# Optimization experiments

Hardware: AMD Instinct MI355X
Metric: run time of the kernel (lower is better)

The kernel has to match this reference:

```python
import jax, jax.numpy as jnp
import numpy as np

N_NODES = 100000
N_EDGES = 3200000
D_IN = 256
D_OUT = 256


def setup_inputs() -> dict:
    key = jax.random.key(0)
    k1, k2, k3, k4, k5 = jax.random.split(key, 5)
    features = jax.random.normal(k1, (N_NODES, D_IN), dtype=jnp.float32)
    # xavier_uniform init for the weight
    limit = np.sqrt(6.0 / (D_IN + D_OUT)).astype(np.float32)
    weight = jax.random.uniform(k2, (D_IN, D_OUT), minval=-limit, maxval=limit, dtype=jnp.float32)
    adj_row = jax.random.randint(k3, (N_EDGES,), 0, N_NODES, dtype=jnp.int64)
    adj_col = jax.random.randint(k4, (N_EDGES,), 0, N_NODES, dtype=jnp.int64)
    adj_val = jax.random.uniform(k5, (N_EDGES,), dtype=jnp.float32)
    return {"features": features, "weight": weight, "adj_row": adj_row,
            "adj_col": adj_col, "adj_val": adj_val}


def reference(features, weight, adj_row, adj_col, adj_val):
    # support = features @ W   (dense GEMM)
    support = features @ weight                      # [N, D_OUT]
    # spmm: out[i] = sum_e val[e] * support[col[e]] for edges with row[e] == i
    gathered = adj_val[:, None] * support[adj_col]   # [E, D_OUT]
    out = jax.ops.segment_sum(gathered, adj_row, num_segments=features.shape[0])
    return jax.nn.relu(out)
```

## Files before the change

kernel.cpp:

```cpp
#include <hip/hip_runtime.h>
#include <hip/hip_bf16.h>

#define N_NODES 100000
#define N_EDGES 3200000
#define NBUCK   391

typedef short v8s __attribute__((ext_vector_type(8)));
typedef float v4f __attribute__((ext_vector_type(4)));

__device__ __forceinline__ unsigned short f2b(float x) {
    __hip_bfloat16 h = __float2bfloat16(x);
    return *reinterpret_cast<unsigned short*>(&h);
}
__device__ __forceinline__ float b2f(unsigned short u) {
    return __uint_as_float(((unsigned int)u) << 16);
}

__device__ __forceinline__ void gld16(const void* g, void* l) {
    __builtin_amdgcn_global_load_lds(
        (const __attribute__((address_space(1))) void*)g,
        (__attribute__((address_space(3))) void*)l, 16, 0, 0);
}

__global__ void transpose_b(const float* __restrict__ B, unsigned short* __restrict__ BT) {
    int n = blockIdx.x;
    int k = threadIdx.x;
    BT[n * 256 + k] = f2b(B[k * 256 + n]);
}

__global__ __launch_bounds__(512)
void gemm_dma(const float* __restrict__ A, const unsigned short* __restrict__ BT,
              unsigned short* __restrict__ C) {
    __shared__ __align__(16) float          sA[128 * 64];
    __shared__ __align__(16) unsigned short sB[256 * 64];

    const int tid  = threadIdx.x;
    const int wave = tid >> 6;
    const int lane = tid & 63;
    const int quad = lane >> 4;
    const int l16  = lane & 15;
    const int row0 = blockIdx.x * 128;

    v4f acc[16];
#pragma unroll
    for (int t = 0; t < 16; t++) acc[t] = (v4f){0.f, 0.f, 0.f, 0.f};

    const int ml = wave * 16 + l16;

    for (int ks = 0; ks < 4; ks++) {
        const int kbase = ks * 64;
#pragma unroll
        for (int i = 0; i < 4; i++) {
            int s = i * 512 + tid;
            int m = s >> 4;
            int c = (s & 15) ^ (m & 15);
            int row = row0 + m;
            if (row >= N_NODES) row = row0;
            gld16(A + (size_t)row * 256 + kbase + c * 4, (char*)sA + (size_t)s * 16);
        }
#pragma unroll
        for (int i = 0; i < 4; i++) {
            int s = i * 512 + tid;
            int n = s >> 3;
            int c = (s & 7) ^ (n & 7);
            gld16(BT + (size_t)n * 256 + kbase + c * 8, (char*)sB + (size_t)s * 16);
        }
        __syncthreads();

#pragma unroll
        for (int sub = 0; sub < 2; sub++) {
            int ca  = sub * 8 + 2 * quad;
            int pa0 = ml * 16 + (ca ^ (ml & 15));
            int pa1 = ml * 16 + ((ca + 1) ^ (ml & 15));
            v4f lo = *(const v4f*)&sA[pa0 * 4];
            v4f hi = *(const v4f*)&sA[pa1 * 4];
            v8s af;
            af[0] = (short)f2b(lo[0]); af[1] = (short)f2b(lo[1]);
            af[2] = (short)f2b(lo[2]); af[3] = (short)f2b(lo[3]);
            af[4] = (short)f2b(hi[0]); af[5] = (short)f2b(hi[1]);
            af[6] = (short)f2b(hi[2]); af[7] = (short)f2b(hi[3]);
            int cb = sub * 4 + quad;
#pragma unroll
            for (int t = 0; t < 16; t++) {
                int n  = t * 16 + l16;
                int pb = n * 8 + (cb ^ (n & 7));
                v8s bf = *(const v8s*)&sB[pb * 8];
                acc[t] = __builtin_amdgcn_mfma_f32_16x16x32_bf16(af, bf, acc[t], 0, 0, 0);
            }
        }
        __syncthreads();
    }

    const int grow_base = row0 + wave * 16 + quad * 4;
#pragma unroll
    for (int t = 0; t < 16; t++) {
#pragma unroll
        for (int r = 0; r < 4; r++) {
            int grow = grow_base + r;
            if (grow < N_NODES)
                C[(size_t)grow * 256 + t * 16 + l16] = f2b(acc[t][r]);
        }
    }
}

__global__ __launch_bounds__(256)
void bhist_kernel(const int* __restrict__ row, int* __restrict__ ghist) {
    __shared__ int h[NBUCK];
    const int tid = threadIdx.x;
    for (int i = tid; i < NBUCK; i += 256) h[i] = 0;
    __syncthreads();
    const int e0 = blockIdx.x * 4096;
#pragma unroll
    for (int j = 0; j < 16; j++) {
        int e = e0 + j * 256 + tid;
        if (e < N_EDGES) atomicAdd(&h[row[e] >> 8], 1);
    }
    __syncthreads();
    for (int i = tid; i < NBUCK; i += 256)
        if (h[i]) atomicAdd(&ghist[i], h[i]);
}

__global__ void bscan_kernel(const int* __restrict__ ghist, int* __restrict__ bbase,
                             int* __restrict__ gcur) {
    __shared__ int s[512];
    const int tid = threadIdx.x;
    int x = (tid < NBUCK) ? ghist[tid] : 0;
    s[tid] = x;
    __syncthreads();
    for (int off = 1; off < 512; off <<= 1) {
        int v = (tid >= off) ? s[tid - off] : 0;
        __syncthreads();
        s[tid] += v;
        __syncthreads();
    }
    if (tid < NBUCK) {
        int b = s[tid] - x;
        bbase[tid] = b;
        gcur[tid]  = b;
    }
}

__global__ __launch_bounds__(256)
void bin_kernel(const int* __restrict__ row, const int* __restrict__ col,
                const float* __restrict__ val, int* __restrict__ gcur,
                int2* __restrict__ bucket) {
    __shared__ int lc[NBUCK];
    const int tid = threadIdx.x;
    const int e0 = blockIdx.x * 4096;
    int r[16], c[16];
    float v[16];
#pragma unroll
    for (int j = 0; j < 16; j++) {
        int e = e0 + j * 256 + tid;
        if (e < N_EDGES) { r[j] = row[e]; c[j] = col[e]; v[j] = val[e]; }
        else r[j] = -1;
    }
    for (int i = tid; i < NBUCK; i += 256) lc[i] = 0;
    __syncthreads();
#pragma unroll
    for (int j = 0; j < 16; j++)
        if (r[j] >= 0) atomicAdd(&lc[r[j] >> 8], 1);
    __syncthreads();
    for (int i = tid; i < NBUCK; i += 256) {
        int cnt = lc[i];
        lc[i] = cnt ? atomicAdd(&gcur[i], cnt) : 0;
    }
    __syncthreads();
#pragma unroll
    for (int j = 0; j < 16; j++) {
        if (r[j] >= 0) {
            int b = r[j] >> 8;
            int p = atomicAdd(&lc[b], 1);
            bucket[p] = make_int2(((r[j] & 255) << 20) | c[j], __float_as_int(v[j]));
        }
    }
}

__global__ __launch_bounds__(256)
void csort_kernel(const int2* __restrict__ bucket, const int* __restrict__ bbase,
                  const int* __restrict__ gcur, unsigned int* __restrict__ csr,
                  int* __restrict__ offs, int* __restrict__ counts) {
    __shared__ int h[256];
    __shared__ int s[256];
    __shared__ int cur[256];
    const int tid  = threadIdx.x;
    const int b    = blockIdx.x;
    const int base = bbase[b];
    const int end  = gcur[b];

    h[tid] = 0;
    __syncthreads();
    for (int i = base + tid; i < end; i += 256)
        atomicAdd(&h[bucket[i].x >> 20], 1);
    __syncthreads();

    int x = h[tid];
    s[tid] = x;
    __syncthreads();
    for (int off = 1; off < 256; off <<= 1) {
        int v2 = (tid >= off) ? s[tid - off] : 0;
        __syncthreads();
        s[tid] += v2;
        __syncthreads();
    }
    int ro = s[tid] - x;
    int grow = b * 256 + tid;
    if (grow < N_NODES) {
        offs[grow]   = base + ro;
        counts[grow] = x;
    }
    cur[tid] = base + ro;
    __syncthreads();

    for (int i = base + tid; i < end; i += 256) {
        int2 w = bucket[i];
        int rl = w.x >> 20;
        int p  = atomicAdd(&cur[rl], 1);
        unsigned int vb = (((unsigned int)w.y + 0x8000u) >> 16) & 0x7FFFu;
        csr[p] = (vb << 17) | (unsigned int)(w.x & 0x1FFFF);
    }
}

__global__ __launch_bounds__(256)
void spmm_kernel(const unsigned short* __restrict__ sup,
                 const int* __restrict__ offs, const int* __restrict__ counts,
                 const unsigned int* __restrict__ csr, float* __restrict__ out) {
    const int wave = threadIdx.x >> 6;
    const int lane = threadIdx.x & 63;
    const int row  = blockIdx.x * 4 + wave;
    if (row >= N_NODES) return;

    const int start = offs[row];
    const int deg   = counts[row];

    float a0 = 0.f, a1 = 0.f, a2 = 0.f, a3 = 0.f;

    for (int base = 0; base < deg; base += 64) {
        int nb = deg - base;
        if (nb > 64) nb = 64;
        int c = 0;
        float v = 0.f;
        if (lane < nb) {
            unsigned int w = csr[start + base + lane];
            c = (int)(w & 0x1FFFFu);
            v = __uint_as_float((w >> 17) << 16);
        }
        int j = 0;
        for (; j + 4 <= nb; j += 4) {
            int   c0 = __shfl(c, j),     c1 = __shfl(c, j + 1);
            int   c2 = __shfl(c, j + 2), c3 = __shfl(c, j + 3);
            float v0 = __shfl(v, j),     v1 = __shfl(v, j + 1);
            float v2 = __shfl(v, j + 2), v3 = __shfl(v, j + 3);
            ushort4 h0 = *(const ushort4*)(sup + (size_t)c0 * 256 + lane * 4);
            ushort4 h1 = *(const ushort4*)(sup + (size_t)c1 * 256 + lane * 4);
            ushort4 h2 = *(const ushort4*)(sup + (size_t)c2 * 256 + lane * 4);
            ushort4 h3 = *(const ushort4*)(sup + (size_t)c3 * 256 + lane * 4);
            a0 += v0 * b2f(h0.x); a1 += v0 * b2f(h0.y);
            a2 += v0 * b2f(h0.z); a3 += v0 * b2f(h0.w);
            a0 += v1 * b2f(h1.x); a1 += v1 * b2f(h1.y);
            a2 += v1 * b2f(h1.z); a3 += v1 * b2f(h1.w);
            a0 += v2 * b2f(h2.x); a1 += v2 * b2f(h2.y);
            a2 += v2 * b2f(h2.z); a3 += v2 * b2f(h2.w);
            a0 += v3 * b2f(h3.x); a1 += v3 * b2f(h3.y);
            a2 += v3 * b2f(h3.z); a3 += v3 * b2f(h3.w);
        }
        for (; j < nb; j++) {
            int   cj = __shfl(c, j);
            float vj = __shfl(v, j);
            ushort4 hh = *(const ushort4*)(sup + (size_t)cj * 256 + lane * 4);
            a0 += vj * b2f(hh.x); a1 += vj * b2f(hh.y);
            a2 += vj * b2f(hh.z); a3 += vj * b2f(hh.w);
        }
    }

    float4 o;
    o.x = a0 > 0.f ? a0 : 0.f;
    o.y = a1 > 0.f ? a1 : 0.f;
    o.z = a2 > 0.f ? a2 : 0.f;
    o.w = a3 > 0.f ? a3 : 0.f;
    *(float4*)(out + (size_t)row * 256 + lane * 4) = o;
}

extern "C" void kernel_launch(void* const* d_in, const int* in_sizes, int n_in,
                              void* d_out, int out_size, void* d_ws, size_t ws_size,
                              hipStream_t stream) {
    const float* features = (const float*)d_in[0];
    const float* weight   = (const float*)d_in[1];
    const int*   adj_row  = (const int*)d_in[2];
    const int*   adj_col  = (const int*)d_in[3];
    const float* adj_val  = (const float*)d_in[4];
    float* out = (float*)d_out;

    char* ws = (char*)d_ws;
    size_t off = 0;
    auto alloc = [&](size_t bytes) -> char* {
        char* p = ws + off;
        off = (off + bytes + 255) & ~(size_t)255;
        return p;
    };
    unsigned short* sup     = (unsigned short*)alloc((size_t)N_NODES * 256 * 2);
    unsigned short* BT      = (unsigned short*)alloc(256 * 256 * 2);
    int*            counts  = (int*)alloc((size_t)N_NODES * 4);
    int*            offsets = (int*)alloc((size_t)N_NODES * 4);
    int*            ghist   = (int*)alloc(512 * 4);
    int*            bbase   = (int*)alloc(512 * 4);
    int*            gcur    = (int*)alloc(512 * 4);
    int2*           bucket  = (int2*)alloc((size_t)N_EDGES * 8);
    unsigned int*   csr     = (unsigned int*)alloc((size_t)N_EDGES * 4);

    hipMemsetAsync(ghist, 0, NBUCK * 4, stream);

    transpose_b<<<256, 256, 0, stream>>>(weight, BT);
    gemm_dma<<<782, 512, 0, stream>>>(features, BT, sup);
    bhist_kernel<<<782, 256, 0, stream>>>(adj_row, ghist);
    bscan_kernel<<<1, 512, 0, stream>>>(ghist, bbase, gcur);
    bin_kernel<<<782, 256, 0, stream>>>(adj_row, adj_col, adj_val, gcur, bucket);
    csort_kernel<<<NBUCK, 256, 0, stream>>>(bucket, bbase, gcur, csr, offsets, counts);
    spmm_kernel<<<25000, 256, 0, stream>>>(sup, offsets, counts, csr, out);
}
```

Measured before the change: 540.0 us.

## Build CSR with direct per-row atomics and scan; unroll SpMM gather by 8

Replaces the two-level bucket sort (bucket histogram, bin into an intermediate int2 buffer, per-bucket counting sort) with a direct per-row global-atomic histogram, a three-kernel prefix scan over row counts, and an atomic scatter straight into the packed CSR array. This drops the 8-byte-per-edge intermediate bucket buffer and one full pass over edges. The cost is heavy global atomic contention on per-row counters and scattered CSR writes. The SpMM inner loop also gains an 8-edge unrolled path so more gathers are in flight per wave, at some register cost.

After: 815.7 us. +51.1%, slower.

```diff
diff --git a/kernel.cpp b/kernel.cpp
--- a/kernel.cpp
+++ b/kernel.cpp
@@ -3,7 +3,7 @@
 
 #define N_NODES 100000
 #define N_EDGES 3200000
-#define NBUCK   391
+#define NBLK_SCAN 98
 
 typedef short v8s __attribute__((ext_vector_type(8)));
 typedef float v4f __attribute__((ext_vector_type(4)));
@@ -104,120 +104,74 @@
 }
 
 __global__ __launch_bounds__(256)
-void bhist_kernel(const int* __restrict__ row, int* __restrict__ ghist) {
-    __shared__ int h[NBUCK];
+void hist_kernel(const int* __restrict__ row, int* __restrict__ counts) {
+    const int e0 = blockIdx.x * 4096 + threadIdx.x;
+#pragma unroll
+    for (int j = 0; j < 16; j++) {
+        int e = e0 + j * 256;
+        if (e < N_EDGES) atomicAdd(&counts[row[e]], 1);
+    }
+}
+
+__global__ __launch_bounds__(1024)
+void scan1_kernel(const int* __restrict__ counts, int* __restrict__ offs,
+                  int* __restrict__ bsum) {
+    __shared__ int s[1024];
     const int tid = threadIdx.x;
-    for (int i = tid; i < NBUCK; i += 256) h[i] = 0;
-    __syncthreads();
-    const int e0 = blockIdx.x * 4096;
-#pragma unroll
-    for (int j = 0; j < 16; j++) {
-        int e = e0 + j * 256 + tid;
-        if (e < N_EDGES) atomicAdd(&h[row[e] >> 8], 1);
-    }
-    __syncthreads();
-    for (int i = tid; i < NBUCK; i += 256)
-        if (h[i]) atomicAdd(&ghist[i], h[i]);
-}
-
-__global__ void bscan_kernel(const int* __restrict__ ghist, int* __restrict__ bbase,
-                             int* __restrict__ gcur) {
-    __shared__ int s[512];
-    const int tid = threadIdx.x;
-    int x = (tid < NBUCK) ? ghist[tid] : 0;
+    const int i = blockIdx.x * 1024 + tid;
+    int x = (i < N_NODES) ? counts[i] : 0;
     s[tid] = x;
     __syncthreads();
-    for (int off = 1; off < 512; off <<= 1) {
+    for (int off = 1; off < 1024; off <<= 1) {
         int v = (tid >= off) ? s[tid - off] : 0;
         __syncthreads();
         s[tid] += v;
         __syncthreads();
     }
-    if (tid < NBUCK) {
-        int b = s[tid] - x;
-        bbase[tid] = b;
-        gcur[tid]  = b;
-    }
-}
-
-__global__ __launch_bounds__(256)
-void bin_kernel(const int* __restrict__ row, const int* __restrict__ col,
-                const float* __restrict__ val, int* __restrict__ gcur,
-                int2* __restrict__ bucket) {
-    __shared__ int lc[NBUCK];
+    if (i < N_NODES) offs[i] = s[tid] - x;
+    if (tid == 1023) bsum[blockIdx.x] = s[1023];
+}
+
+__global__ void scan2_kernel(int* __restrict__ bsum) {
+    __shared__ int s[128];
     const int tid = threadIdx.x;
-    const int e0 = blockIdx.x * 4096;
-    int r[16], c[16];
-    float v[16];
-#pragma unroll
-    for (int j = 0; j < 16; j++) {
-        int e = e0 + j * 256 + tid;
-        if (e < N_EDGES) { r[j] = row[e]; c[j] = col[e]; v[j] = val[e]; }
-        else r[j] = -1;
-    }
-    for (int i = tid; i < NBUCK; i += 256) lc[i] = 0;
-    __syncthreads();
-#pragma unroll
-    for (int j = 0; j < 16; j++)
-        if (r[j] >= 0) atomicAdd(&lc[r[j] >> 8], 1);
-    __syncthreads();
-    for (int i = tid; i < NBUCK; i += 256) {
-        int cnt = lc[i];
-        lc[i] = cnt ? atomicAdd(&gcur[i], cnt) : 0;
-    }
-    __syncthreads();
-#pragma unroll
-    for (int j = 0; j < 16; j++) {
-        if (r[j] >= 0) {
-            int b = r[j] >> 8;
-            int p = atomicAdd(&lc[b], 1);
-            bucket[p] = make_int2(((r[j] & 255) << 20) | c[j], __float_as_int(v[j]));
-        }
-    }
-}
-
-__global__ __launch_bounds__(256)
-void csort_kernel(const int2* __restrict__ bucket, const int* __restrict__ bbase,
-                  const int* __restrict__ gcur, unsigned int* __restrict__ csr,
-                  int* __restrict__ offs, int* __restrict__ counts) {
-    __shared__ int h[256];
-    __shared__ int s[256];
-    __shared__ int cur[256];
-    const int tid  = threadIdx.x;
-    const int b    = blockIdx.x;
-    const int base = bbase[b];
-    const int end  = gcur[b];
-
-    h[tid] = 0;
-    __syncthreads();
-    for (int i = base + tid; i < end; i += 256)
-        atomicAdd(&h[bucket[i].x >> 20], 1);
-    __syncthreads();
-
-    int x = h[tid];
+    int x = (tid < NBLK_SCAN) ? bsum[tid] : 0;
     s[tid] = x;
     __syncthreads();
-    for (int off = 1; off < 256; off <<= 1) {
-        int v2 = (tid >= off) ? s[tid - off] : 0;
-        __syncthreads();
-        s[tid] += v2;
-        __syncthreads();
-    }
-    int ro = s[tid] - x;
-    int grow = b * 256 + tid;
-    if (grow < N_NODES) {
-        offs[grow]   = base + ro;
-        counts[grow] = x;
-    }
-    cur[tid] = base + ro;
-    __syncthreads();
-
-    for (int i = base + tid; i < end; i += 256) {
-        int2 w = bucket[i];
-        int rl = w.x >> 20;
-        int p  = atomicAdd(&cur[rl], 1);
-        unsigned int vb = (((unsigned int)w.y + 0x8000u) >> 16) & 0x7FFFu;
-        csr[p] = (vb << 17) | (unsigned int)(w.x & 0x1FFFF);
+    for (int off = 1; off < 128; off <<= 1) {
+        int v = (tid >= off) ? s[tid - off] : 0;
+        __syncthreads();
+        s[tid] += v;
+        __syncthreads();
+    }
+    if (tid < NBLK_SCAN) bsum[tid] = s[tid] - x;
+}
+
+__global__ __launch_bounds__(256)
+void fixup_kernel(int* __restrict__ offs, const int* __restrict__ bsum,
+                  int* __restrict__ cur) {
+    const int i = blockIdx.x * 256 + threadIdx.x;
+    if (i < N_NODES) {
+        int o = offs[i] + bsum[i >> 10];
+        offs[i] = o;
+        cur[i]  = o;
+    }
+}
+
+__global__ __launch_bounds__(256)
+void scatter_kernel(const int* __restrict__ row, const int* __restrict__ col,
+                    const float* __restrict__ val, int* __restrict__ cur,
+                    unsigned int* __restrict__ csr) {
+    const int e0 = blockIdx.x * 4096 + threadIdx.x;
+#pragma unroll
+    for (int j = 0; j < 16; j++) {
+        int e = e0 + j * 256;
+        if (e < N_EDGES) {
+            int r = row[e];
+            int p = atomicAdd(&cur[r], 1);
+            unsigned int vb = (((unsigned int)__float_as_int(val[e]) + 0x8000u) >> 16) & 0x7FFFu;
+            csr[p] = (vb << 17) | (unsigned int)col[e];
+        }
     }
 }
 
@@ -246,6 +200,21 @@
             v = __uint_as_float((w >> 17) << 16);
         }
         int j = 0;
+        for (; j + 8 <= nb; j += 8) {
+            int   cc[8];
+            float vv[8];
+#pragma unroll
+            for (int u = 0; u < 8; u++) { cc[u] = __shfl(c, j + u); vv[u] = __shfl(v, j + u); }
+            ushort4 h[8];
+#pragma unroll
+            for (int u = 0; u < 8; u++)
+                h[u] = *(const ushort4*)(sup + (size_t)cc[u] * 256 + lane * 4);
+#pragma unroll
+            for (int u = 0; u < 8; u++) {
+                a0 += vv[u] * b2f(h[u].x); a1 += vv[u] * b2f(h[u].y);
+                a2 += vv[u] * b2f(h[u].z); a3 += vv[u] * b2f(h[u].w);
+            }
+        }
         for (; j + 4 <= nb; j += 4) {
             int   c0 = __shfl(c, j),     c1 = __shfl(c, j + 1);
             int   c2 = __shfl(c, j + 2), c3 = __shfl(c, j + 3);
@@ -302,19 +271,18 @@
     unsigned short* BT      = (unsigned short*)alloc(256 * 256 * 2);
     int*            counts  = (int*)alloc((size_t)N_NODES * 4);
     int*            offsets = (int*)alloc((size_t)N_NODES * 4);
-    int*            ghist   = (int*)alloc(512 * 4);
-    int*            bbase   = (int*)alloc(512 * 4);
-    int*            gcur    = (int*)alloc(512 * 4);
-    int2*           bucket  = (int2*)alloc((size_t)N_EDGES * 8);
+    int*            cur     = (int*)alloc((size_t)N_NODES * 4);
+    int*            bsum    = (int*)alloc(512 * 4);
     unsigned int*   csr     = (unsigned int*)alloc((size_t)N_EDGES * 4);
 
-    hipMemsetAsync(ghist, 0, NBUCK * 4, stream);
+    hipMemsetAsync(counts, 0, (size_t)N_NODES * 4, stream);
 
     transpose_b<<<256, 256, 0, stream>>>(weight, BT);
     gemm_dma<<<782, 512, 0, stream>>>(features, BT, sup);
-    bhist_kernel<<<782, 256, 0, stream>>>(adj_row, ghist);
-    bscan_kernel<<<1, 512, 0, stream>>>(ghist, bbase, gcur);
-    bin_kernel<<<782, 256, 0, stream>>>(adj_row, adj_col, adj_val, gcur, bucket);
-    csort_kernel<<<NBUCK, 256, 0, stream>>>(bucket, bbase, gcur, csr, offsets, counts);
+    hist_kernel<<<782, 256, 0, stream>>>(adj_row, counts);
+    scan1_kernel<<<NBLK_SCAN, 1024, 0, stream>>>(counts, offsets, bsum);
+    scan2_kernel<<<1, 128, 0, stream>>>(bsum);
+    fixup_kernel<<<391, 256, 0, stream>>>(offsets, bsum, cur);
+    scatter_kernel<<<782, 256, 0, stream>>>(adj_row, adj_col, adj_val, cur, csr);
     spmm_kernel<<<25000, 256, 0, stream>>>(sup, offsets, counts, csr, out);
 }
```

## Stage bucketed edges in LDS for grouped scatter, widen csort, unroll spmm by 8

Applied to the files above, without the earlier changes.

The binning kernel now sorts each block's 4096 edges by bucket in shared memory with a local prefix scan, then writes them out in bucket order. Consecutive threads therefore hit contiguous bucket ranges instead of scattering one edge at a time. The csort kernel moves to 512 threads per block, and the spmm inner loop gains an 8-way unrolled gather path to keep more loads in flight. The cost is extra shared memory and syncs in the binning kernel (about 50KB per block, which lowers occupancy), plus more register pressure in spmm.

New measurement: 511.0 us. 1.06x faster.

```diff
diff --git a/kernel.cpp b/kernel.cpp
--- a/kernel.cpp
+++ b/kernel.cpp
@@ -140,79 +140,111 @@
     }
 }
 
-__global__ __launch_bounds__(256)
-void bin_kernel(const int* __restrict__ row, const int* __restrict__ col,
-                const float* __restrict__ val, int* __restrict__ gcur,
-                int2* __restrict__ bucket) {
-    __shared__ int lc[NBUCK];
+__global__ __launch_bounds__(512)
+void bin2_kernel(const int* __restrict__ row, const int* __restrict__ col,
+                 const float* __restrict__ val, int* __restrict__ gcur,
+                 int2* __restrict__ bucket) {
+    __shared__ int  cnt[512];
+    __shared__ int  ls[512];
+    __shared__ int  gb[512];
+    __shared__ int  lcur[512];
+    __shared__ __align__(16) int2 stage[4096];
+    __shared__ int  gdst[4096];
+
     const int tid = threadIdx.x;
-    const int e0 = blockIdx.x * 4096;
-    int r[16], c[16];
-    float v[16];
-#pragma unroll
-    for (int j = 0; j < 16; j++) {
-        int e = e0 + j * 256 + tid;
+    const int e0  = blockIdx.x * 4096;
+
+    int r[8], c[8];
+    float v[8];
+#pragma unroll
+    for (int j = 0; j < 8; j++) {
+        int e = e0 + j * 512 + tid;
         if (e < N_EDGES) { r[j] = row[e]; c[j] = col[e]; v[j] = val[e]; }
         else r[j] = -1;
     }
-    for (int i = tid; i < NBUCK; i += 256) lc[i] = 0;
-    __syncthreads();
-#pragma unroll
-    for (int j = 0; j < 16; j++)
-        if (r[j] >= 0) atomicAdd(&lc[r[j] >> 8], 1);
-    __syncthreads();
-    for (int i = tid; i < NBUCK; i += 256) {
-        int cnt = lc[i];
-        lc[i] = cnt ? atomicAdd(&gcur[i], cnt) : 0;
-    }
-    __syncthreads();
-#pragma unroll
-    for (int j = 0; j < 16; j++) {
+
+    cnt[tid] = 0;
+    __syncthreads();
+#pragma unroll
+    for (int j = 0; j < 8; j++)
+        if (r[j] >= 0) atomicAdd(&cnt[r[j] >> 8], 1);
+    __syncthreads();
+
+    int x = cnt[tid];
+    int gbase = 0;
+    if (x) gbase = atomicAdd(&gcur[tid], x);
+    gb[tid] = gbase;
+
+    lcur[tid] = x;
+    __syncthreads();
+    for (int off = 1; off < 512; off <<= 1) {
+        int t = (tid >= off) ? lcur[tid - off] : 0;
+        __syncthreads();
+        lcur[tid] += t;
+        __syncthreads();
+    }
+    int excl = lcur[tid] - x;
+    __syncthreads();
+    ls[tid]   = excl;
+    lcur[tid] = excl;
+    __syncthreads();
+
+#pragma unroll
+    for (int j = 0; j < 8; j++) {
         if (r[j] >= 0) {
             int b = r[j] >> 8;
-            int p = atomicAdd(&lc[b], 1);
-            bucket[p] = make_int2(((r[j] & 255) << 20) | c[j], __float_as_int(v[j]));
-        }
-    }
-}
-
-__global__ __launch_bounds__(256)
+            int q = atomicAdd(&lcur[b], 1);
+            stage[q] = make_int2(((r[j] & 255) << 20) | c[j], __float_as_int(v[j]));
+            gdst[q]  = gb[b] + (q - ls[b]);
+        }
+    }
+    __syncthreads();
+
+    int tot = N_EDGES - e0;
+    if (tot > 4096) tot = 4096;
+    for (int i = tid; i < tot; i += 512)
+        bucket[gdst[i]] = stage[i];
+}
+
+__global__ __launch_bounds__(512)
 void csort_kernel(const int2* __restrict__ bucket, const int* __restrict__ bbase,
                   const int* __restrict__ gcur, unsigned int* __restrict__ csr,
                   int* __restrict__ offs, int* __restrict__ counts) {
     __shared__ int h[256];
-    __shared__ int s[256];
+    __shared__ int s[512];
     __shared__ int cur[256];
     const int tid  = threadIdx.x;
     const int b    = blockIdx.x;
     const int base = bbase[b];
     const int end  = gcur[b];
 
-    h[tid] = 0;
-    __syncthreads();
-    for (int i = base + tid; i < end; i += 256)
+    if (tid < 256) h[tid] = 0;
+    __syncthreads();
+    for (int i = base + tid; i < end; i += 512)
         atomicAdd(&h[bucket[i].x >> 20], 1);
     __syncthreads();
 
-    int x = h[tid];
+    int x = (tid < 256) ? h[tid] : 0;
     s[tid] = x;
     __syncthreads();
-    for (int off = 1; off < 256; off <<= 1) {
+    for (int off = 1; off < 512; off <<= 1) {
         int v2 = (tid >= off) ? s[tid - off] : 0;
         __syncthreads();
         s[tid] += v2;
         __syncthreads();
     }
-    int ro = s[tid] - x;
-    int grow = b * 256 + tid;
-    if (grow < N_NODES) {
-        offs[grow]   = base + ro;
-        counts[grow] = x;
-    }
-    cur[tid] = base + ro;
-    __syncthreads();
-
-    for (int i = base + tid; i < end; i += 256) {
+    if (tid < 256) {
+        int ro = s[tid] - x;
+        int grow = b * 256 + tid;
+        if (grow < N_NODES) {
+            offs[grow]   = base + ro;
+            counts[grow] = x;
+        }
+        cur[tid] = base + ro;
+    }
+    __syncthreads();
+
+    for (int i = base + tid; i < end; i += 512) {
         int2 w = bucket[i];
         int rl = w.x >> 20;
         int p  = atomicAdd(&cur[rl], 1);
@@ -246,6 +278,21 @@
             v = __uint_as_float((w >> 17) << 16);
         }
         int j = 0;
+        for (; j + 8 <= nb; j += 8) {
+            int   cc[8];
+            float vv[8];
+#pragma unroll
+            for (int u = 0; u < 8; u++) { cc[u] = __shfl(c, j + u); vv[u] = __shfl(v, j + u); }
+            ushort4 h[8];
+#pragma unroll
+            for (int u = 0; u < 8; u++)
+                h[u] = *(const ushort4*)(sup + (size_t)cc[u] * 256 + lane * 4);
+#pragma unroll
+            for (int u = 0; u < 8; u++) {
+                a0 += vv[u] * b2f(h[u].x); a1 += vv[u] * b2f(h[u].y);
+                a2 += vv[u] * b2f(h[u].z); a3 += vv[u] * b2f(h[u].w);
+            }
+        }
         for (; j + 4 <= nb; j += 4) {
             int   c0 = __shfl(c, j),     c1 = __shfl(c, j + 1);
             int   c2 = __shfl(c, j + 2), c3 = __shfl(c, j + 3);
@@ -308,13 +355,13 @@
     int2*           bucket  = (int2*)alloc((size_t)N_EDGES * 8);
     unsigned int*   csr     = (unsigned int*)alloc((size_t)N_EDGES * 4);
 
-    hipMemsetAsync(ghist, 0, NBUCK * 4, stream);
+    hipMemsetAsync(ghist, 0, 512 * 4, stream);
 
     transpose_b<<<256, 256, 0, stream>>>(weight, BT);
     gemm_dma<<<782, 512, 0, stream>>>(features, BT, sup);
     bhist_kernel<<<782, 256, 0, stream>>>(adj_row, ghist);
     bscan_kernel<<<1, 512, 0, stream>>>(ghist, bbase, gcur);
-    bin_kernel<<<782, 256, 0, stream>>>(adj_row, adj_col, adj_val, gcur, bucket);
-    csort_kernel<<<NBUCK, 256, 0, stream>>>(bucket, bbase, gcur, csr, offsets, counts);
+    bin2_kernel<<<782, 512, 0, stream>>>(adj_row, adj_col, adj_val, gcur, bucket);
+    csort_kernel<<<NBUCK, 512, 0, stream>>>(bucket, bbase, gcur, csr, offsets, counts);
     spmm_kernel<<<25000, 256, 0, stream>>>(sup, offsets, counts, csr, out);
 }
```
